# Optimization experiments

Measured on AMD Instinct MI355X. Metric: run time of the kernel, lower is better.

Reference implementation:

```python
import jax, jax.numpy as jnp
import numpy as np

VOCAB = 32000
D = 512
H = 8
B = 1
SEQ = 4096
CHUNK = 1024  # max_len == chunk size


def _pe(seq, d):
    pos = np.arange(seq, dtype=np.float32)[:, None]
    div = np.exp(np.arange(0, d, 2, dtype=np.float32) * (-np.log(10000.0) / d))
    pe = np.zeros((seq, d), dtype=np.float32)
    pe[:, 0::2] = np.sin(pos * div)
    pe[:, 1::2] = np.cos(pos * div)
    return jnp.asarray(pe)


def _mha(x, w_in, b_in, w_out, b_out, h):
    # x: (..., L, d); attention along L, batched over leading dims.
    lead = x.shape[:-2]
    L, d = x.shape[-2], x.shape[-1]
    hd = d // h
    qkv = x @ w_in.T + b_in                      # (..., L, 3d)
    q, k, v = jnp.split(qkv, 3, axis=-1)
    q = q.reshape(lead + (L, h, hd))
    k = k.reshape(lead + (L, h, hd))
    v = v.reshape(lead + (L, h, hd))
    scores = jnp.einsum('...qhd,...khd->...hqk', q, k) * (1.0 / np.sqrt(hd))
    attn = jax.nn.softmax(scores, axis=-1)
    o = jnp.einsum('...hqk,...khd->...qhd', attn, v).reshape(lead + (L, d))
    return o @ w_out.T + b_out


def _ln(x, g, b, eps=1e-5):
    m = x.mean(-1, keepdims=True)
    v = x.var(-1, keepdims=True)
    return (x - m) / jnp.sqrt(v + eps) * g + b


def setup_inputs() -> dict:
    key = jax.random.key(0)
    ks = jax.random.split(key, 10)
    n = lambda k, s: jax.random.normal(k, s, jnp.float32) * 0.02
    return {
        'tokens': jax.random.randint(ks[0], (B, SEQ), 0, VOCAB),
        'emb': n(ks[1], (VOCAB, D)),
        'chunk_w_in': n(ks[2], (3 * D, D)), 'chunk_b_in': jnp.zeros((3 * D,), jnp.float32),
        'chunk_w_out': n(ks[3], (D, D)), 'chunk_b_out': jnp.zeros((D,), jnp.float32),
        'glob_w_in': n(ks[4], (3 * D, D)), 'glob_b_in': jnp.zeros((3 * D,), jnp.float32),
        'glob_w_out': n(ks[5], (D, D)), 'glob_b_out': jnp.zeros((D,), jnp.float32),
        'ln1_g': jnp.ones((D,), jnp.float32), 'ln1_b': jnp.zeros((D,), jnp.float32),
        'ffn_w1': n(ks[6], (4 * D, D)), 'ffn_b1': jnp.zeros((4 * D,), jnp.float32),
        'ffn_w2': n(ks[7], (D, 4 * D)), 'ffn_b2': jnp.zeros((D,), jnp.float32),
        'ln2_g': jnp.ones((D,), jnp.float32), 'ln2_b': jnp.zeros((D,), jnp.float32),
        'fc_w': n(ks[8], (VOCAB, D)), 'fc_b': jnp.zeros((VOCAB,), jnp.float32),
    }


def reference(tokens, emb, chunk_w_in, chunk_b_in, chunk_w_out, chunk_b_out,
              glob_w_in, glob_b_in, glob_w_out, glob_b_out,
              ln1_g, ln1_b, ffn_w1, ffn_b1, ffn_w2, ffn_b2,
              ln2_g, ln2_b, fc_w, fc_b):
    # embedding * sqrt(d) + sinusoidal positional encoding (dropout in eval = identity)
    x = emb[tokens] * np.sqrt(D).astype(np.float32) + _pe(SEQ, D)[None]  # (B, S, d)
    b, s, d = x.shape
    nc = s // CHUNK
    # BeamSplitter chunk stage: attend across the nc chunks at each intra-chunk position
    xc = x.reshape(b, nc, CHUNK, d).transpose(0, 2, 1, 3)   # (B, CHUNK, nc, d)
    ca = _mha(xc, chunk_w_in, chunk_b_in, chunk_w_out, chunk_b_out, H)
    ca = ca.transpose(0, 2, 1, 3).reshape(b, s, d)          # (B, S, d)
    # global stage: full attention over the sequence
    ga = _mha(ca, glob_w_in, glob_b_in, glob_w_out, glob_b_out, H)
    # post-norm transformer encoder layer
    x = _ln(x + ga, ln1_g, ln1_b)
    f = jax.nn.relu(x @ ffn_w1.T + ffn_b1) @ ffn_w2.T + ffn_b2
    x = _ln(x + f, ln2_g, ln2_b)
    return x @ fc_w.T + fc_b                                 # (B, S, VOCAB)
```

## Files before the change

### kernel.cpp

```cpp
#include <hip/hip_runtime.h>

typedef __attribute__((ext_vector_type(8))) short bf16x8;
typedef __attribute__((ext_vector_type(4))) float f32x4;
typedef unsigned short u16;

__device__ __forceinline__ u16 f2b(float f) {
  union { float f; unsigned u; } v; v.f = f;
  return (u16)((v.u + 0x7FFFu + ((v.u >> 16) & 1u)) >> 16);
}
__device__ __forceinline__ float b2f(u16 x) {
  union { unsigned u; float f; } v; v.u = (unsigned)x << 16; return v.f;
}

__device__ __forceinline__ void gload16(const void* g, void* l) {
  __builtin_amdgcn_global_load_lds((__attribute__((address_space(1))) void*)(g),
                                   (__attribute__((address_space(3))) void*)(l),
                                   16, 0, 0);
}

__device__ __forceinline__ void mbar() {
  asm volatile("" ::: "memory");
  __builtin_amdgcn_s_barrier();
  asm volatile("" ::: "memory");
}

__device__ __forceinline__ void cv1(const float4* __restrict__ s, u16* __restrict__ d, int i) {
  float4 v = s[i];
  unsigned long long pk = (unsigned long long)f2b(v.x) |
                          ((unsigned long long)f2b(v.y) << 16) |
                          ((unsigned long long)f2b(v.z) << 32) |
                          ((unsigned long long)f2b(v.w) << 48);
  *(unsigned long long*)(d + (size_t)i * 4) = pk;
}

__global__ __launch_bounds__(256)
void f2b_multi(const float4* s0, u16* d0, const float4* s1, u16* d1,
               const float4* s2, u16* d2, const float4* s3, u16* d3,
               const float4* s4, u16* d4, const float4* s5, u16* d5,
               const float4* s6, u16* d6) {
  int i = blockIdx.x * 256 + threadIdx.x;
  const int stride = gridDim.x * 256;
  for (; i < 5144576; i += stride) {
    int j = i;
    if (j < 196608) { cv1(s0, d0, j); continue; }
    j -= 196608;
    if (j < 65536) { cv1(s1, d1, j); continue; }
    j -= 65536;
    if (j < 196608) { cv1(s2, d2, j); continue; }
    j -= 196608;
    if (j < 65536) { cv1(s3, d3, j); continue; }
    j -= 65536;
    if (j < 262144) { cv1(s4, d4, j); continue; }
    j -= 262144;
    if (j < 262144) { cv1(s5, d5, j); continue; }
    j -= 262144;
    cv1(s6, d6, j);
  }
}

__global__ __launch_bounds__(256) void embed_pe(const int* __restrict__ tok,
    const float* __restrict__ emb, float* __restrict__ xf, u16* __restrict__ xb) {
  const int s = blockIdx.x;
  const int i = threadIdx.x;
  const int t = tok[s];
  const float div = __expf((float)(2 * i) * -0.017988946039015984f);
  const float ang = (float)s * div;
  const float sv = sinf(ang), cv = cosf(ang);
  const float* e = emb + (size_t)t * 512 + 2 * i;
  const float x0 = e[0] * 22.627416997969522f + sv;
  const float x1 = e[1] * 22.627416997969522f + cv;
  const size_t o = (size_t)s * 512 + 2 * i;
  xf[o] = x0; xf[o + 1] = x1;
  xb[o] = f2b(x0); xb[o + 1] = f2b(x1);
}

template<int BM, int RELU, int WF32, int WB16>
__global__ __launch_bounds__(256)
void gemm_bt(const u16* __restrict__ A, const u16* __restrict__ B,
             const float* __restrict__ bias, float* __restrict__ Cf,
             u16* __restrict__ Cb, int M, int N, int K)
{
  constexpr int MFR = BM / 32;
  __shared__ __align__(16) u16 As[BM * 32];
  __shared__ __align__(16) u16 Bs[128 * 32];
  const int tid = threadIdx.x;
  const int wid = tid >> 6, lane = tid & 63;
  const int lo = lane & 15, hi = lane >> 4;
  const int nbn = N >> 7;
  const int cpx = (int)gridDim.x >> 3;
  const int bid = blockIdx.x;
  const int swz = (bid & 7) * cpx + (bid >> 3);
  const int bi = swz / nbn, bj = swz - bi * nbn;
  const size_t row0 = (size_t)bi * BM, col0 = (size_t)bj << 7;
  const int wr = (wid >> 1) * (BM / 2), wc = (wid & 1) << 6;
  const int r0 = (wid << 5) + (lane >> 2);
  const int c0 = (lane & 3) << 3;
  const int ra = tid >> 2, ca = (tid & 3) << 3;

  f32x4 acc[MFR][4] = {};

  for (int k0 = 0; k0 < K; k0 += 32) {
    __syncthreads();
    if constexpr (BM == 128) {
      gload16(A + (row0 + r0) * (size_t)K + k0 + c0,      &As[wid * 1024]);
      gload16(A + (row0 + r0 + 16) * (size_t)K + k0 + c0, &As[wid * 1024 + 512]);
    } else {
      gload16(A + (row0 + ra) * (size_t)K + k0 + ca,      &As[wid * 512]);
    }
    gload16(B + (col0 + r0) * (size_t)K + k0 + c0,      &Bs[wid * 1024]);
    gload16(B + (col0 + r0 + 16) * (size_t)K + k0 + c0, &Bs[wid * 1024 + 512]);
    __syncthreads();
    bf16x8 af[MFR], bfr[4];
#pragma unroll
    for (int m = 0; m < MFR; ++m)
      af[m] = *(const bf16x8*)&As[(wr + m * 16 + lo) * 32 + hi * 8];
#pragma unroll
    for (int n = 0; n < 4; ++n)
      bfr[n] = *(const bf16x8*)&Bs[(wc + n * 16 + lo) * 32 + hi * 8];
#pragma unroll
    for (int m = 0; m < MFR; ++m)
#pragma unroll
      for (int n = 0; n < 4; ++n)
        acc[m][n] = __builtin_amdgcn_mfma_f32_16x16x32_bf16(af[m], bfr[n], acc[m][n], 0, 0, 0);
  }

#pragma unroll
  for (int m = 0; m < MFR; ++m)
#pragma unroll
    for (int n = 0; n < 4; ++n) {
      const size_t c = col0 + wc + n * 16 + lo;
      const float bv = bias[c];
#pragma unroll
      for (int i = 0; i < 4; ++i) {
        const size_t r = row0 + wr + m * 16 + hi * 4 + i;
        float v = acc[m][n][i] + bv;
        if (RELU) v = fmaxf(v, 0.0f);
        if (WF32) Cf[r * (size_t)N + c] = v;
        if (WB16) Cb[r * (size_t)N + c] = f2b(v);
      }
    }
}

template<int KC>
__global__ __launch_bounds__(512, 2)
void gemm256(const u16* __restrict__ A, const u16* __restrict__ B,
             const float* __restrict__ bias, float* __restrict__ C,
             int M, int N)
{
  constexpr int T = KC / 64;
  __shared__ __align__(16) u16 LA[2][256 * 64];
  __shared__ __align__(16) u16 LB[2][256 * 64];
  const int tid = threadIdx.x;
  const int wid = tid >> 6, lane = tid & 63;
  const int lo = lane & 15, hi = lane >> 4;
  const int nbn = N >> 8;
  const int cpx = (int)gridDim.x >> 3;
  const int bid = blockIdx.x;
  const int swz = (bid & 7) * cpx + (bid >> 3);
  const int bi = swz / nbn, bj = swz - bi * nbn;
  const size_t row0 = (size_t)bi << 8, col0 = (size_t)bj << 8;
  const int wrow = (wid >> 2) << 7;
  const int wcol = (wid & 3) << 6;

  const int srow = (wid << 3) + (lane >> 3);
  const int scol = ((lane & 7) ^ (lane >> 3)) << 3;
  const u16* srcA = A + (row0 + srow) * (size_t)KC + scol;
  const u16* srcB = B + (col0 + srow) * (size_t)KC + scol;
  const int ldst = wid << 9;

  f32x4 acc[8][4] = {};

  auto stage = [&](int t, int b) {
    const size_t ko = (size_t)t * 64;
#pragma unroll
    for (int i = 0; i < 4; ++i)
      gload16(srcA + ko + (size_t)(i * 64) * KC, &LA[b][ldst + i * 4096]);
#pragma unroll
    for (int i = 0; i < 4; ++i)
      gload16(srcB + ko + (size_t)(i * 64) * KC, &LB[b][ldst + i * 4096]);
  };

  auto rd = [&](const u16* base, int row, int ks) -> bf16x8 {
    const int byte = row * 128 + ((((ks << 2) | hi) ^ (row & 7)) << 4);
    return *(const bf16x8*)((const char*)base + byte);
  };

  stage(0, 0);
  stage(1, 1);

  for (int t = 0; t < T; ++t) {
    const int b = t & 1;
    const u16* Ab = LA[b];
    const u16* Bb = LB[b];
    if (t + 1 < T) { asm volatile("s_waitcnt vmcnt(8)" ::: "memory"); }
    else           { asm volatile("s_waitcnt vmcnt(0)" ::: "memory"); }
    __builtin_amdgcn_sched_barrier(0);
    mbar();

    bf16x8 afr[4], bfr[4];
#pragma unroll
    for (int ks = 0; ks < 2; ++ks) {
#pragma unroll
      for (int m = 0; m < 4; ++m) afr[m] = rd(Ab, wrow + m * 16 + lo, ks);
#pragma unroll
      for (int n = 0; n < 4; ++n) bfr[n] = rd(Bb, wcol + n * 16 + lo, ks);
      mbar();
      asm volatile("s_waitcnt lgkmcnt(0)" ::: "memory");
      __builtin_amdgcn_sched_barrier(0);
      __builtin_amdgcn_s_setprio(1);
#pragma unroll
      for (int m = 0; m < 4; ++m)
#pragma unroll
        for (int n = 0; n < 4; ++n)
          acc[m][n] = __builtin_amdgcn_mfma_f32_16x16x32_bf16(afr[m], bfr[n], acc[m][n], 0, 0, 0);
      __builtin_amdgcn_s_setprio(0);
      mbar();
#pragma unroll
      for (int m = 0; m < 4; ++m) afr[m] = rd(Ab, wrow + (4 + m) * 16 + lo, ks);
      mbar();
      asm volatile("s_waitcnt lgkmcnt(0)" ::: "memory");
      __builtin_amdgcn_sched_barrier(0);
      __builtin_amdgcn_s_setprio(1);
#pragma unroll
      for (int m = 0; m < 4; ++m)
#pragma unroll
        for (int n = 0; n < 4; ++n)
          acc[4 + m][n] = __builtin_amdgcn_mfma_f32_16x16x32_bf16(afr[m], bfr[n], acc[4 + m][n], 0, 0, 0);
      __builtin_amdgcn_s_setprio(0);
      mbar();
    }
    if (t + 2 < T) stage(t + 2, b);
  }

#pragma unroll
  for (int m = 0; m < 8; ++m)
#pragma unroll
    for (int n = 0; n < 4; ++n) {
      const size_t c = col0 + wcol + n * 16 + lo;
      const float bv = bias[c];
#pragma unroll
      for (int i = 0; i < 4; ++i) {
        const size_t r = row0 + wrow + m * 16 + hi * 4 + i;
        C[r * (size_t)N + c] = acc[m][n][i] + bv;
      }
    }
}

__global__ __launch_bounds__(64)
void chunk_attn(const u16* __restrict__ qkv, u16* __restrict__ out) {
  const int p = blockIdx.x, h = blockIdx.y, d = threadIdx.x;
  float q[4], k[4], v[4];
#pragma unroll
  for (int c = 0; c < 4; ++c) {
    const u16* b = qkv + (size_t)((c << 10) + p) * 1536 + (h << 6) + d;
    q[c] = b2f(b[0]); k[c] = b2f(b[512]); v[c] = b2f(b[1024]);
  }
  float sc[4][4];
#pragma unroll
  for (int i = 0; i < 4; ++i)
#pragma unroll
    for (int j = 0; j < 4; ++j) sc[i][j] = q[i] * k[j];
#pragma unroll
  for (int mask = 1; mask < 64; mask <<= 1)
#pragma unroll
    for (int i = 0; i < 4; ++i)
#pragma unroll
      for (int j = 0; j < 4; ++j) sc[i][j] += __shfl_xor(sc[i][j], mask);
#pragma unroll
  for (int i = 0; i < 4; ++i) {
    float s0 = sc[i][0] * 0.125f, s1 = sc[i][1] * 0.125f,
          s2 = sc[i][2] * 0.125f, s3 = sc[i][3] * 0.125f;
    const float mx = fmaxf(fmaxf(s0, s1), fmaxf(s2, s3));
    const float e0 = __expf(s0 - mx), e1 = __expf(s1 - mx),
                e2 = __expf(s2 - mx), e3 = __expf(s3 - mx);
    const float inv = 1.0f / (e0 + e1 + e2 + e3);
    const float o = (e0 * v[0] + e1 * v[1] + e2 * v[2] + e3 * v[3]) * inv;
    out[(size_t)((i << 10) + p) * 512 + (h << 6) + d] = f2b(o);
  }
}

__global__ __launch_bounds__(512)
void flash_attn(const u16* __restrict__ qkv, u16* __restrict__ out) {
  __shared__ __align__(16) u16 Ks[64 * 64];
  __shared__ __align__(16) u16 Vt[64 * 64];
  __shared__ __align__(16) u16 Pp[8][16 * 64];
  const int tid = threadIdx.x, wid = tid >> 6, lane = tid & 63;
  const int lo = lane & 15, hi = lane >> 4;
  const int q0 = blockIdx.x << 7, h = blockIdx.y;
  const int hoff = h << 6;
  char* KsB = (char*)Ks; char* VtB = (char*)Vt;
  char* Pw = (char*)&Pp[wid][0];
  const int xsw = (lo & 7) << 4;

  bf16x8 qf[2];
#pragma unroll
  for (int kh = 0; kh < 2; ++kh)
    qf[kh] = *(const bf16x8*)(qkv + (size_t)(q0 + wid * 16 + lo) * 1536 + hoff + kh * 32 + hi * 8);

  f32x4 o[4] = {};
  float mr = -3e38f, lr = 0.f;

  const int krow = tid >> 3, kq = tid & 7;

  bf16x8 kpre = *(const bf16x8*)(qkv + (size_t)krow * 1536 + 512 + hoff + kq * 8);
  bf16x8 vpre = *(const bf16x8*)(qkv + (size_t)krow * 1536 + 1024 + hoff + kq * 8);

  for (int kv0 = 0; kv0 < 4096; kv0 += 64) {
    __syncthreads();
    *(bf16x8*)(KsB + ((krow * 128 + kq * 16) ^ ((krow & 7) << 4))) = kpre;
#pragma unroll
    for (int dd = 0; dd < 8; ++dd) {
      const int d = kq * 8 + dd;
      *(u16*)(VtB + ((d * 128 + 2 * krow) ^ ((d & 7) << 4))) = (u16)vpre[dd];
    }
    __syncthreads();
    if (kv0 + 64 < 4096) {
      kpre = *(const bf16x8*)(qkv + (size_t)(kv0 + 64 + krow) * 1536 + 512 + hoff + kq * 8);
      vpre = *(const bf16x8*)(qkv + (size_t)(kv0 + 64 + krow) * 1536 + 1024 + hoff + kq * 8);
    }

    f32x4 s[4] = {};
#pragma unroll
    for (int n = 0; n < 4; ++n) {
      const int key = n * 16 + lo;
#pragma unroll
      for (int kh = 0; kh < 2; ++kh) {
        bf16x8 kf = *(const bf16x8*)(KsB + ((key * 128 + kh * 64 + hi * 16) ^ ((key & 7) << 4)));
        s[n] = __builtin_amdgcn_mfma_f32_16x16x32_bf16(kf, qf[kh], s[n], 0, 0, 0);
      }
      s[n] *= 0.125f;
    }

    float pm = s[0][0];
#pragma unroll
    for (int n = 0; n < 4; ++n)
#pragma unroll
      for (int i = 0; i < 4; ++i) pm = fmaxf(pm, s[n][i]);
    pm = fmaxf(pm, __shfl_xor(pm, 16));
    pm = fmaxf(pm, __shfl_xor(pm, 32));

    if (__any(pm > mr + 8.f)) {
      const float mn = fmaxf(mr, pm);
      const float sc = __expf(mr - mn);
      mr = mn;
      lr *= sc;
#pragma unroll
      for (int i = 0; i < 4; ++i) {
        const float sq = __shfl(sc, hi * 4 + i);
#pragma unroll
        for (int n = 0; n < 4; ++n) o[n][i] *= sq;
      }
    }

    float rs = 0.f;
    unsigned U[8];
#pragma unroll
    for (int n = 0; n < 4; ++n) {
      const float p0 = __expf(s[n][0] - mr);
      const float p1 = __expf(s[n][1] - mr);
      const float p2 = __expf(s[n][2] - mr);
      const float p3 = __expf(s[n][3] - mr);
      rs += (p0 + p1) + (p2 + p3);
      asm("v_cvt_pk_bf16_f32 %0, %1, %2" : "=v"(U[2 * n])     : "v"(p0), "v"(p1));
      asm("v_cvt_pk_bf16_f32 %0, %1, %2" : "=v"(U[2 * n + 1]) : "v"(p2), "v"(p3));
    }
    rs += __shfl_xor(rs, 16);
    rs += __shfl_xor(rs, 32);
    lr += rs;
#pragma unroll
    for (int n = 0; n < 4; ++n) {
      const int off = lo * 128 + ((n * 32 + hi * 8) ^ xsw);
      const unsigned long long dw = (unsigned long long)U[2 * n] |
                                    ((unsigned long long)U[2 * n + 1] << 32);
      *(unsigned long long*)(Pw + off) = dw;
    }

#pragma unroll
    for (int kh = 0; kh < 2; ++kh) {
      bf16x8 pa = *(const bf16x8*)(Pw + lo * 128 + ((kh * 64 + hi * 16) ^ xsw));
#pragma unroll
      for (int n = 0; n < 4; ++n) {
        const int vd = n * 16 + lo;
        bf16x8 vf = *(const bf16x8*)(VtB + ((vd * 128 + kh * 64 + hi * 16) ^ ((vd & 7) << 4)));
        o[n] = __builtin_amdgcn_mfma_f32_16x16x32_bf16(pa, vf, o[n], 0, 0, 0);
      }
    }
  }

#pragma unroll
  for (int i = 0; i < 4; ++i) {
    const float lq = __shfl(lr, hi * 4 + i);
    const float inv = 1.0f / lq;
    const int r = q0 + wid * 16 + hi * 4 + i;
#pragma unroll
    for (int n = 0; n < 4; ++n)
      out[(size_t)r * 512 + hoff + n * 16 + lo] = f2b(o[n][i] * inv);
  }
}

__global__ __launch_bounds__(256)
void add_ln(const float* __restrict__ a, const float* __restrict__ b,
            const float* __restrict__ g, const float* __restrict__ be,
            float* __restrict__ of, u16* __restrict__ ob) {
  const int wid = threadIdx.x >> 6, lane = threadIdx.x & 63;
  const int row = blockIdx.x * 4 + wid;
  const size_t base = (size_t)row * 512 + lane * 8;
  float4 a0 = *(const float4*)(a + base), a1 = *(const float4*)(a + base + 4);
  float4 b0 = *(const float4*)(b + base), b1 = *(const float4*)(b + base + 4);
  float x[8] = {a0.x + b0.x, a0.y + b0.y, a0.z + b0.z, a0.w + b0.w,
                a1.x + b1.x, a1.y + b1.y, a1.z + b1.z, a1.w + b1.w};
  float s = 0.f, sq = 0.f;
#pragma unroll
  for (int j = 0; j < 8; ++j) { s += x[j]; sq += x[j] * x[j]; }
#pragma unroll
  for (int mask = 1; mask < 64; mask <<= 1) {
    s += __shfl_xor(s, mask);
    sq += __shfl_xor(sq, mask);
  }
  const float mean = s * (1.0f / 512.0f);
  const float var = sq * (1.0f / 512.0f) - mean * mean;
  const float rstd = rsqrtf(var + 1e-5f);
  float4 g0 = *(const float4*)(g + lane * 8), g1 = *(const float4*)(g + lane * 8 + 4);
  float4 e0 = *(const float4*)(be + lane * 8), e1 = *(const float4*)(be + lane * 8 + 4);
  const float gg[8] = {g0.x, g0.y, g0.z, g0.w, g1.x, g1.y, g1.z, g1.w};
  const float bb[8] = {e0.x, e0.y, e0.z, e0.w, e1.x, e1.y, e1.z, e1.w};
#pragma unroll
  for (int j = 0; j < 8; ++j) {
    const float y = (x[j] - mean) * rstd * gg[j] + bb[j];
    of[base + j] = y;
    ob[base + j] = f2b(y);
  }
}

extern "C" void kernel_launch(void* const* d_in, const int* in_sizes, int n_in,
                              void* d_out, int out_size, void* d_ws, size_t ws_size,
                              hipStream_t stream) {
  (void)in_sizes; (void)n_in; (void)out_size; (void)ws_size;
  const int*   tokens = (const int*)d_in[0];
  const float* emb    = (const float*)d_in[1];
  const float* cwin   = (const float*)d_in[2];
  const float* cbin   = (const float*)d_in[3];
  const float* cwout  = (const float*)d_in[4];
  const float* cbout  = (const float*)d_in[5];
  const float* gwin   = (const float*)d_in[6];
  const float* gbin   = (const float*)d_in[7];
  const float* gwout  = (const float*)d_in[8];
  const float* gbout  = (const float*)d_in[9];
  const float* ln1g   = (const float*)d_in[10];
  const float* ln1b   = (const float*)d_in[11];
  const float* fw1    = (const float*)d_in[12];
  const float* fb1    = (const float*)d_in[13];
  const float* fw2    = (const float*)d_in[14];
  const float* fb2    = (const float*)d_in[15];
  const float* ln2g   = (const float*)d_in[16];
  const float* ln2b   = (const float*)d_in[17];
  const float* fcw    = (const float*)d_in[18];
  const float* fcb    = (const float*)d_in[19];
  float* out = (float*)d_out;

  char* ws = (char*)d_ws;
  size_t off = 0;
  auto alloc = [&](size_t bytes) -> void* {
    void* p = ws + off;
    off += (bytes + 255) & ~(size_t)255;
    return p;
  };
  u16*   xb    = (u16*)alloc((size_t)4096 * 512 * 2);
  float* xf    = (float*)alloc((size_t)4096 * 512 * 4);
  u16*   qkv1b = (u16*)alloc((size_t)4096 * 1536 * 2);
  u16*   at1   = (u16*)alloc((size_t)4096 * 512 * 2);
  u16*   cab   = (u16*)alloc((size_t)4096 * 512 * 2);
  u16*   qkv2  = (u16*)alloc((size_t)4096 * 1536 * 2);
  u16*   at2   = (u16*)alloc((size_t)4096 * 512 * 2);
  float* gaf   = (float*)alloc((size_t)4096 * 512 * 4);
  float* x1f   = (float*)alloc((size_t)4096 * 512 * 4);
  u16*   x1b   = (u16*)alloc((size_t)4096 * 512 * 2);
  u16*   f1b   = (u16*)alloc((size_t)4096 * 2048 * 2);
  float* ff    = (float*)alloc((size_t)4096 * 512 * 4);
  float* x2f   = (float*)alloc((size_t)4096 * 512 * 4);
  u16*   x2b   = (u16*)alloc((size_t)4096 * 512 * 2);
  u16*   wcinb  = (u16*)alloc((size_t)1536 * 512 * 2);
  u16*   wcoutb = (u16*)alloc((size_t)512 * 512 * 2);
  u16*   wginb  = (u16*)alloc((size_t)1536 * 512 * 2);
  u16*   wgoutb = (u16*)alloc((size_t)512 * 512 * 2);
  u16*   wf1b   = (u16*)alloc((size_t)2048 * 512 * 2);
  u16*   wf2b   = (u16*)alloc((size_t)512 * 2048 * 2);
  u16*   wfcb   = (u16*)alloc((size_t)32000 * 512 * 2);

  f2b_multi<<<2048, 256, 0, stream>>>(
      (const float4*)cwin, wcinb, (const float4*)cwout, wcoutb,
      (const float4*)gwin, wginb, (const float4*)gwout, wgoutb,
      (const float4*)fw1, wf1b, (const float4*)fw2, wf2b,
      (const float4*)fcw, wfcb);

  embed_pe<<<4096, 256, 0, stream>>>(tokens, emb, xf, xb);

  gemm_bt<128, 0, 0, 1><<<384, 256, 0, stream>>>(xb, wcinb, cbin, (float*)nullptr, qkv1b, 4096, 1536, 512);
  chunk_attn<<<dim3(1024, 8), 64, 0, stream>>>(qkv1b, at1);
  gemm_bt<64, 0, 0, 1><<<256, 256, 0, stream>>>(at1, wcoutb, cbout, (float*)nullptr, cab, 4096, 512, 512);

  gemm_bt<128, 0, 0, 1><<<384, 256, 0, stream>>>(cab, wginb, gbin, (float*)nullptr, qkv2, 4096, 1536, 512);
  flash_attn<<<dim3(32, 8), 512, 0, stream>>>(qkv2, at2);
  gemm_bt<64, 0, 1, 0><<<256, 256, 0, stream>>>(at2, wgoutb, gbout, gaf, (u16*)nullptr, 4096, 512, 512);

  add_ln<<<1024, 256, 0, stream>>>(xf, gaf, ln1g, ln1b, x1f, x1b);
  gemm_bt<128, 1, 0, 1><<<512, 256, 0, stream>>>(x1b, wf1b, fb1, (float*)nullptr, f1b, 4096, 2048, 512);
  gemm_bt<64, 0, 1, 0><<<256, 256, 0, stream>>>(f1b, wf2b, fb2, ff, (u16*)nullptr, 4096, 512, 2048);
  add_ln<<<1024, 256, 0, stream>>>(x1f, ff, ln2g, ln2b, x2f, x2b);

  gemm256<512><<<2000, 512, 0, stream>>>(x2b, wfcb, fcb, out, 4096, 32000);
}
```

Before: 484.0 us.

## Deepen GEMM K-tile with swizzled LDS, pack V transpose, fold softmax scale into exp2

The GEMM main loop now stages 64-wide K tiles through XOR-swizzled LDS, which halves barrier rounds and reduces bank conflicts on the fragment reads. In flash attention, the V transpose into LDS uses a lane shuffle to pair rows, so each thread writes four 32-bit words instead of eight 16-bit stores. The 1/sqrt(d) scale and log2(e) are folded into a single FMA feeding exp2, and the lazy-rescale threshold is raised to match the unscaled scores. The costs are more LDS per GEMM block, which may lower occupancy, and extra shuffle work in the transpose.

```diff
diff --git a/kernel.cpp b/kernel.cpp
--- a/kernel.cpp
+++ b/kernel.cpp
@@ -81,8 +81,8 @@
              u16* __restrict__ Cb, int M, int N, int K)
 {
   constexpr int MFR = BM / 32;
-  __shared__ __align__(16) u16 As[BM * 32];
-  __shared__ __align__(16) u16 Bs[128 * 32];
+  __shared__ __align__(16) u16 As[BM * 64];
+  __shared__ __align__(16) u16 Bs[128 * 64];
   const int tid = threadIdx.x;
   const int wid = tid >> 6, lane = tid & 63;
   const int lo = lane & 15, hi = lane >> 4;
@@ -93,35 +93,40 @@
   const int bi = swz / nbn, bj = swz - bi * nbn;
   const size_t row0 = (size_t)bi * BM, col0 = (size_t)bj << 7;
   const int wr = (wid >> 1) * (BM / 2), wc = (wid & 1) << 6;
-  const int r0 = (wid << 5) + (lane >> 2);
-  const int c0 = (lane & 3) << 3;
-  const int ra = tid >> 2, ca = (tid & 3) << 3;
+  const int srow = (wid << 3) + (lane >> 3);
+  const int scol = ((lane & 7) ^ (lane >> 3)) << 3;
 
   f32x4 acc[MFR][4] = {};
 
-  for (int k0 = 0; k0 < K; k0 += 32) {
+  auto rdA = [&](int row, int ks) -> bf16x8 {
+    return *(const bf16x8*)((const char*)As + row * 128 + ((((ks << 2) | hi) ^ (row & 7)) << 4));
+  };
+  auto rdB = [&](int row, int ks) -> bf16x8 {
+    return *(const bf16x8*)((const char*)Bs + row * 128 + ((((ks << 2) | hi) ^ (row & 7)) << 4));
+  };
+
+  for (int k0 = 0; k0 < K; k0 += 64) {
     __syncthreads();
-    if constexpr (BM == 128) {
-      gload16(A + (row0 + r0) * (size_t)K + k0 + c0,      &As[wid * 1024]);
-      gload16(A + (row0 + r0 + 16) * (size_t)K + k0 + c0, &As[wid * 1024 + 512]);
-    } else {
-      gload16(A + (row0 + ra) * (size_t)K + k0 + ca,      &As[wid * 512]);
-    }
-    gload16(B + (col0 + r0) * (size_t)K + k0 + c0,      &Bs[wid * 1024]);
-    gload16(B + (col0 + r0 + 16) * (size_t)K + k0 + c0, &Bs[wid * 1024 + 512]);
+#pragma unroll
+    for (int p = 0; p < BM / 32; ++p)
+      gload16(A + (row0 + srow + 32 * p) * (size_t)K + k0 + scol, &As[(wid * 8 + 32 * p) * 64]);
+#pragma unroll
+    for (int p = 0; p < 4; ++p)
+      gload16(B + (col0 + srow + 32 * p) * (size_t)K + k0 + scol, &Bs[(wid * 8 + 32 * p) * 64]);
     __syncthreads();
-    bf16x8 af[MFR], bfr[4];
-#pragma unroll
-    for (int m = 0; m < MFR; ++m)
-      af[m] = *(const bf16x8*)&As[(wr + m * 16 + lo) * 32 + hi * 8];
-#pragma unroll
-    for (int n = 0; n < 4; ++n)
-      bfr[n] = *(const bf16x8*)&Bs[(wc + n * 16 + lo) * 32 + hi * 8];
-#pragma unroll
-    for (int m = 0; m < MFR; ++m)
-#pragma unroll
-      for (int n = 0; n < 4; ++n)
-        acc[m][n] = __builtin_amdgcn_mfma_f32_16x16x32_bf16(af[m], bfr[n], acc[m][n], 0, 0, 0);
+#pragma unroll
+    for (int ks = 0; ks < 2; ++ks) {
+      bf16x8 af[MFR], bfr[4];
+#pragma unroll
+      for (int m = 0; m < MFR; ++m) af[m] = rdA(wr + m * 16 + lo, ks);
+#pragma unroll
+      for (int n = 0; n < 4; ++n) bfr[n] = rdB(wc + n * 16 + lo, ks);
+#pragma unroll
+      for (int m = 0; m < MFR; ++m)
+#pragma unroll
+        for (int n = 0; n < 4; ++n)
+          acc[m][n] = __builtin_amdgcn_mfma_f32_16x16x32_bf16(af[m], bfr[n], acc[m][n], 0, 0, 0);
+    }
   }
 
 #pragma unroll
@@ -291,6 +296,7 @@
   char* KsB = (char*)Ks; char* VtB = (char*)Vt;
   char* Pw = (char*)&Pp[wid][0];
   const int xsw = (lo & 7) << 4;
+  constexpr float C1 = 0.18033688011112042f;
 
   bf16x8 qf[2];
 #pragma unroll
@@ -308,10 +314,27 @@
   for (int kv0 = 0; kv0 < 4096; kv0 += 64) {
     __syncthreads();
     *(bf16x8*)(KsB + ((krow * 128 + kq * 16) ^ ((krow & 7) << 4))) = kpre;
-#pragma unroll
-    for (int dd = 0; dd < 8; ++dd) {
-      const int d = kq * 8 + dd;
-      *(u16*)(VtB + ((d * 128 + 2 * krow) ^ ((d & 7) << 4))) = (u16)vpre[dd];
+    {
+      const unsigned* vp = (const unsigned*)&vpre;
+      const int oddr = krow & 1;
+      const unsigned t0 = oddr ? vp[0] : vp[2];
+      const unsigned t1 = oddr ? vp[1] : vp[3];
+      const unsigned r0 = (unsigned)__shfl_xor((int)t0, 8);
+      const unsigned r1 = (unsigned)__shfl_xor((int)t1, 8);
+      const unsigned E0 = oddr ? r0 : vp[0];
+      const unsigned E1 = oddr ? r1 : vp[1];
+      const unsigned O0 = oddr ? vp[2] : r0;
+      const unsigned O1 = oddr ? vp[3] : r1;
+      const int jp = krow & ~1;
+      const int db = kq * 8 + oddr * 4;
+      unsigned w0 = (E0 & 0xffffu) | (O0 << 16);
+      unsigned w1 = (E0 >> 16) | (O0 & 0xffff0000u);
+      unsigned w2 = (E1 & 0xffffu) | (O1 << 16);
+      unsigned w3 = (E1 >> 16) | (O1 & 0xffff0000u);
+      *(unsigned*)(VtB + (((db + 0) * 128 + 2 * jp) ^ (((db + 0) & 7) << 4))) = w0;
+      *(unsigned*)(VtB + (((db + 1) * 128 + 2 * jp) ^ (((db + 1) & 7) << 4))) = w1;
+      *(unsigned*)(VtB + (((db + 2) * 128 + 2 * jp) ^ (((db + 2) & 7) << 4))) = w2;
+      *(unsigned*)(VtB + (((db + 3) * 128 + 2 * jp) ^ (((db + 3) & 7) << 4))) = w3;
     }
     __syncthreads();
     if (kv0 + 64 < 4096) {
@@ -328,7 +351,6 @@
         bf16x8 kf = *(const bf16x8*)(KsB + ((key * 128 + kh * 64 + hi * 16) ^ ((key & 7) << 4)));
         s[n] = __builtin_amdgcn_mfma_f32_16x16x32_bf16(kf, qf[kh], s[n], 0, 0, 0);
       }
-      s[n] *= 0.125f;
     }
 
     float pm = s[0][0];
@@ -339,9 +361,9 @@
     pm = fmaxf(pm, __shfl_xor(pm, 16));
     pm = fmaxf(pm, __shfl_xor(pm, 32));
 
-    if (__any(pm > mr + 8.f)) {
+    if (__any(pm > mr + 64.f)) {
       const float mn = fmaxf(mr, pm);
-      const float sc = __expf(mr - mn);
+      const float sc = exp2f((mr - mn) * C1);
       mr = mn;
       lr *= sc;
 #pragma unroll
@@ -352,14 +374,15 @@
       }
     }
 
+    const float mc = mr * C1;
     float rs = 0.f;
     unsigned U[8];
 #pragma unroll
     for (int n = 0; n < 4; ++n) {
-      const float p0 = __expf(s[n][0] - mr);
-      const float p1 = __expf(s[n][1] - mr);
-      const float p2 = __expf(s[n][2] - mr);
-      const float p3 = __expf(s[n][3] - mr);
+      const float p0 = exp2f(fmaf(s[n][0], C1, -mc));
+      const float p1 = exp2f(fmaf(s[n][1], C1, -mc));
+      const float p2 = exp2f(fmaf(s[n][2], C1, -mc));
+      const float p3 = exp2f(fmaf(s[n][3], C1, -mc));
       rs += (p0 + p1) + (p2 + p3);
       asm("v_cvt_pk_bf16_f32 %0, %1, %2" : "=v"(U[2 * n])     : "v"(p0), "v"(p1));
       asm("v_cvt_pk_bf16_f32 %0, %1, %2" : "=v"(U[2 * n + 1]) : "v"(p2), "v"(p3));
```

Measured after the change: 474.1 us. -2.0%, faster.
